# Kernel tuning notes

Measured on AMD Instinct MI355X. Metric: run time of the kernel, lower is better.

## Reference

```python
import jax, jax.numpy as jnp
import numpy as np

EMBED_DIM = 512
N_HEADS = 8
HEAD_DIM = EMBED_DIM // N_HEADS
B, S = 4, 2048

def gelu(x):
    # torch F.gelu default = exact erf gelu
    return jax.nn.gelu(x, approximate=False)

def setup_inputs() -> dict:
    key = jax.random.key(0)
    ks = jax.random.split(key, 9)
    sc = 1.0 / np.sqrt(EMBED_DIM)
    inp = {
        'x':   jax.random.normal(ks[0], (B, S, EMBED_DIM), dtype=jnp.float32),
        'Wq':  jax.random.uniform(ks[1], (EMBED_DIM, EMBED_DIM), jnp.float32, -sc, sc),
        'bq':  jax.random.uniform(ks[2], (EMBED_DIM,), jnp.float32, -sc, sc),
        'Wk':  jax.random.uniform(ks[3], (EMBED_DIM, EMBED_DIM), jnp.float32, -sc, sc),
        'bk':  jax.random.uniform(ks[4], (EMBED_DIM,), jnp.float32, -sc, sc),
        'Wv':  jax.random.uniform(ks[5], (EMBED_DIM, EMBED_DIM), jnp.float32, -sc, sc),
        'bv':  jax.random.uniform(ks[6], (EMBED_DIM,), jnp.float32, -sc, sc),
        'Wo':  jax.random.uniform(ks[7], (EMBED_DIM, EMBED_DIM), jnp.float32, -sc, sc),
        'bo':  jax.random.uniform(ks[8], (EMBED_DIM,), jnp.float32, -sc, sc),
    }
    return inp

def reference(x, Wq, bq, Wk, bk, Wv, bv, Wo, bo):
    Bsz, Ssz, _ = x.shape
    def proj(W, b):
        # [B,S,E] -> [B,H,S,D], GELU applied before head split (same math either way)
        h = gelu(jnp.einsum('bse,ef->bsf', x, W.T) + b)
        return h.reshape(Bsz, Ssz, N_HEADS, HEAD_DIM).transpose(0, 2, 1, 3)
    q = proj(Wq, bq)
    k = proj(Wk, bk)
    v = proj(Wv, bv)
    attn = jnp.einsum('bhid,bhjd->bhij', q, k) / np.sqrt(HEAD_DIM).astype(np.float32)
    attn = jax.nn.softmax(attn, axis=-1)
    o = jnp.einsum('bhij,bhjd->bhid', attn, v)
    o = o.transpose(0, 2, 1, 3).reshape(Bsz, Ssz, EMBED_DIM)
    return gelu(jnp.einsum('bse,ef->bsf', o, Wo.T) + bo)
```

## Files before the change

kernel.cpp:

```cpp
#include <hip/hip_runtime.h>
#include <hip/hip_bf16.h>

typedef __bf16 bf16_t;
typedef __bf16 bf16x4 __attribute__((ext_vector_type(4)));
typedef __bf16 bf16x8 __attribute__((ext_vector_type(8)));
typedef float  f32x4  __attribute__((ext_vector_type(4)));
typedef float  f32x8  __attribute__((ext_vector_type(8)));

#define EMBED 512
#define NH    8
#define HD    64
#define SEQ   2048
#define MTOT  8192
#define SCQ   0.18033688011112042f

__device__ __forceinline__ float gelu_f(float x) {
    return 0.5f * x * (1.0f + erff(x * 0.7071067811865475f));
}

__device__ __forceinline__ f32x4 mfma16(bf16x8 a, bf16x8 b, f32x4 c) {
    return __builtin_amdgcn_mfma_f32_16x16x32_bf16(a, b, c, 0, 0, 0);
}

__global__ __launch_bounds__(256)
void convert_kernel(const float* __restrict__ x,  const float* __restrict__ Wq,
                    const float* __restrict__ Wk, const float* __restrict__ Wv,
                    bf16_t* __restrict__ xb, bf16_t* __restrict__ wb)
{
    const int y = blockIdx.y;
    const float* src; bf16_t* dst;
    if (y < 16)      { src = x + (size_t)y * 262144; dst = xb + (size_t)y * 262144; }
    else if (y == 16){ src = Wq; dst = wb; }
    else if (y == 17){ src = Wk; dst = wb + 262144; }
    else             { src = Wv; dst = wb + 524288; }
    const int base = (blockIdx.x * 256 + threadIdx.x) * 16;
    const f32x8 a = *(const f32x8*)(src + base);
    const f32x8 b = *(const f32x8*)(src + base + 8);
    *(bf16x8*)(dst + base)     = __builtin_convertvector(a, bf16x8);
    *(bf16x8*)(dst + base + 8) = __builtin_convertvector(b, bf16x8);
}

template<int MODE, int NTILE>
__global__ __launch_bounds__(256, 3)
void gemm_gelu_kernel(const bf16_t* __restrict__ Xb,
                      const bf16_t* __restrict__ Wb,
                      const float*  __restrict__ Wf,
                      const float*  __restrict__ Bq, const float* __restrict__ Bk,
                      const float*  __restrict__ Bv,
                      bf16_t* __restrict__ O0, bf16_t* __restrict__ O1,
                      bf16_t* __restrict__ O2, float* __restrict__ Of)
{
    constexpr int NTN = NTILE / 32;
    __shared__ __align__(16) bf16_t As[128 * 72];
    __shared__ __align__(16) bf16_t Bs[NTILE * 72];
    const int tid  = threadIdx.x;
    const int lane = tid & 63, w = tid >> 6, quad = lane >> 4, l15 = lane & 15;
    const int m0 = blockIdx.x * 128;
    int mat, n0;
    if (MODE == 0) { mat = blockIdx.y >> 2; n0 = (blockIdx.y & 3) * NTILE; }
    else           { mat = 0;               n0 = blockIdx.y * NTILE; }
    const bf16_t* W  = (MODE == 0) ? (Wb + (size_t)mat * 262144) : nullptr;
    const float*  Bi = (MODE == 1) ? Bq : (mat == 0 ? Bq : (mat == 1 ? Bk : Bv));

    const int wr = (w >> 1) * 64;
    const int wc = (w & 1) * (NTILE / 2);

    const int srow = tid >> 3, scol = (tid & 7) * 8;

    f32x4 acc[4][NTN];
#pragma unroll
    for (int a = 0; a < 4; ++a)
#pragma unroll
        for (int b = 0; b < NTN; ++b) acc[a][b] = f32x4{0.f, 0.f, 0.f, 0.f};

    bf16x8 xp[4];
    bf16x8 wpb[NTN];
    f32x8  wpf[NTN];

#pragma unroll
    for (int it = 0; it < 4; ++it)
        xp[it] = *(const bf16x8*)(Xb + (size_t)(m0 + it * 32 + srow) * EMBED + scol);
#pragma unroll
    for (int it = 0; it < NTN; ++it) {
        const int r = it * 32 + srow;
        if (MODE == 0) wpb[it] = *(const bf16x8*)(W + (size_t)(n0 + r) * EMBED + scol);
        else           wpf[it] = *(const f32x8*)(Wf + (size_t)(n0 + r) * EMBED + scol);
    }

#pragma unroll 1
    for (int kt = 0; kt < 8; ++kt) {
        __syncthreads();
#pragma unroll
        for (int it = 0; it < 4; ++it)
            *(bf16x8*)(As + (it * 32 + srow) * 72 + scol) = xp[it];
#pragma unroll
        for (int it = 0; it < NTN; ++it) {
            const int r = it * 32 + srow;
            if (MODE == 0) *(bf16x8*)(Bs + r * 72 + scol) = wpb[it];
            else *(bf16x8*)(Bs + r * 72 + scol) = __builtin_convertvector(wpf[it], bf16x8);
        }
        if (kt < 7) {
            const int k1 = (kt + 1) * 64;
#pragma unroll
            for (int it = 0; it < 4; ++it)
                xp[it] = *(const bf16x8*)(Xb + (size_t)(m0 + it * 32 + srow) * EMBED + k1 + scol);
#pragma unroll
            for (int it = 0; it < NTN; ++it) {
                const int r = it * 32 + srow;
                if (MODE == 0) wpb[it] = *(const bf16x8*)(W + (size_t)(n0 + r) * EMBED + k1 + scol);
                else           wpf[it] = *(const f32x8*)(Wf + (size_t)(n0 + r) * EMBED + k1 + scol);
            }
        }
        __syncthreads();
#pragma unroll
        for (int ks = 0; ks < 2; ++ks) {
            const int ko = (ks * 4 + quad) * 8;
            bf16x8 av[4], bv[NTN];
#pragma unroll
            for (int mt = 0; mt < 4; ++mt)
                av[mt] = *(const bf16x8*)(As + (wr + mt * 16 + l15) * 72 + ko);
#pragma unroll
            for (int nt = 0; nt < NTN; ++nt)
                bv[nt] = *(const bf16x8*)(Bs + (wc + nt * 16 + l15) * 72 + ko);
#pragma unroll
            for (int mt = 0; mt < 4; ++mt)
#pragma unroll
                for (int nt = 0; nt < NTN; ++nt)
                    acc[mt][nt] = mfma16(av[mt], bv[nt], acc[mt][nt]);
        }
    }

    float biasv[NTN];
#pragma unroll
    for (int nt = 0; nt < NTN; ++nt)
        biasv[nt] = Bi[n0 + wc + nt * 16 + l15];
#pragma unroll
    for (int mt = 0; mt < 4; ++mt) {
        const int mb = m0 + wr + mt * 16 + quad * 4;
        const int bb = mb >> 11, s0 = mb & (SEQ - 1);
#pragma unroll
        for (int nt = 0; nt < NTN; ++nt) {
            const int fc = n0 + wc + nt * 16 + l15;
            const int h = fc >> 6, d = fc & 63;
            float vv[4];
#pragma unroll
            for (int i = 0; i < 4; ++i) vv[i] = gelu_f(acc[mt][nt][i] + biasv[nt]);
            if (MODE == 1) {
#pragma unroll
                for (int i = 0; i < 4; ++i) Of[(size_t)(mb + i) * EMBED + fc] = vv[i];
            } else if (mat == 0) {
#pragma unroll
                for (int i = 0; i < 4; ++i)
                    O0[(((size_t)(bb * NH + h)) * SEQ + s0 + i) * HD + d] = (bf16_t)(vv[i] * SCQ);
            } else if (mat == 1) {
#pragma unroll
                for (int i = 0; i < 4; ++i)
                    O1[(((size_t)(bb * NH + h)) * SEQ + s0 + i) * HD + d] = (bf16_t)vv[i];
            } else {
                bf16x4 pk;
#pragma unroll
                for (int i = 0; i < 4; ++i) pk[i] = (bf16_t)vv[i];
                *(bf16x4*)(O2 + ((size_t)(bb * NH + h) * HD + d) * SEQ + s0) = pk;
            }
        }
    }
}

__global__ __launch_bounds__(256, 3)
void flash_attn_kernel(const bf16_t* __restrict__ Q,
                       const bf16_t* __restrict__ K,
                       const bf16_t* __restrict__ Vt,
                       bf16_t* __restrict__ Og)
{
    __shared__ __align__(16) bf16_t Ks[2][64 * 72];
    __shared__ __align__(16) bf16_t Vs[2][64 * 72];
    __shared__ __align__(16) bf16_t Ps[4][16 * 72];

    const int tid  = threadIdx.x;
    const int lane = tid & 63, w = tid >> 6, quad = lane >> 4, l15 = lane & 15;
    const int bh = blockIdx.y;
    const int q0 = blockIdx.x * 64;
    const size_t baseQK = (size_t)bh * SEQ * HD;
    const size_t baseV  = (size_t)bh * HD * SEQ;
    const int wm = w * 16;

    bf16x8 qf[2];
#pragma unroll
    for (int ks = 0; ks < 2; ++ks)
        qf[ks] = *(const bf16x8*)(Q + baseQK + (size_t)(q0 + wm + l15) * HD + ks * 32 + quad * 8);

    float lsum = 0.f;
    f32x4 oacc[4];
#pragma unroll
    for (int nt = 0; nt < 4; ++nt) oacc[nt] = f32x4{0.f, 0.f, 0.f, 0.f};

    bf16_t* Pw = Ps[w];
    const int r0 = tid >> 3, c0 = (tid & 7) * 8;
    bf16x8 kr0, kr1, vr0, vr1;

    kr0 = *(const bf16x8*)(K + baseQK + (size_t)r0 * HD + c0);
    kr1 = *(const bf16x8*)(K + baseQK + (size_t)(r0 + 32) * HD + c0);
    vr0 = *(const bf16x8*)(Vt + baseV + (size_t)r0 * SEQ + c0);
    vr1 = *(const bf16x8*)(Vt + baseV + (size_t)(r0 + 32) * SEQ + c0);
    *(bf16x8*)(Ks[0] + r0 * 72 + c0)        = kr0;
    *(bf16x8*)(Ks[0] + (r0 + 32) * 72 + c0) = kr1;
    *(bf16x8*)(Vs[0] + r0 * 72 + c0)        = vr0;
    *(bf16x8*)(Vs[0] + (r0 + 32) * 72 + c0) = vr1;
    kr0 = *(const bf16x8*)(K + baseQK + (size_t)(64 + r0) * HD + c0);
    kr1 = *(const bf16x8*)(K + baseQK + (size_t)(64 + r0 + 32) * HD + c0);
    vr0 = *(const bf16x8*)(Vt + baseV + (size_t)r0 * SEQ + 64 + c0);
    vr1 = *(const bf16x8*)(Vt + baseV + (size_t)(r0 + 32) * SEQ + 64 + c0);

#pragma unroll 1
    for (int t = 0; t < 32; ++t) {
        __syncthreads();
        if (t + 1 < 32) {
            bf16_t* Kn = Ks[(t + 1) & 1];
            bf16_t* Vn = Vs[(t + 1) & 1];
            *(bf16x8*)(Kn + r0 * 72 + c0)        = kr0;
            *(bf16x8*)(Kn + (r0 + 32) * 72 + c0) = kr1;
            *(bf16x8*)(Vn + r0 * 72 + c0)        = vr0;
            *(bf16x8*)(Vn + (r0 + 32) * 72 + c0) = vr1;
        }
        if (t + 2 < 32) {
            const int kv = (t + 2) * 64;
            kr0 = *(const bf16x8*)(K + baseQK + (size_t)(kv + r0) * HD + c0);
            kr1 = *(const bf16x8*)(K + baseQK + (size_t)(kv + r0 + 32) * HD + c0);
            vr0 = *(const bf16x8*)(Vt + baseV + (size_t)r0 * SEQ + kv + c0);
            vr1 = *(const bf16x8*)(Vt + baseV + (size_t)(r0 + 32) * SEQ + kv + c0);
        }

        const bf16_t* Kb = Ks[t & 1];
        const bf16_t* Vb = Vs[t & 1];

        f32x4 sf[4];
#pragma unroll
        for (int jt = 0; jt < 4; ++jt) sf[jt] = f32x4{0.f, 0.f, 0.f, 0.f};
#pragma unroll
        for (int ks = 0; ks < 2; ++ks) {
            const int ko = ks * 32 + quad * 8;
#pragma unroll
            for (int jt = 0; jt < 4; ++jt) {
                const bf16x8 a = *(const bf16x8*)(Kb + (jt * 16 + l15) * 72 + ko);
                sf[jt] = mfma16(a, qf[ks], sf[jt]);
            }
        }

#pragma unroll
        for (int jt = 0; jt < 4; ++jt) {
#pragma unroll
            for (int i = 0; i < 4; ++i) {
                const float pv = exp2f(sf[jt][i] - 8.f);
                sf[jt][i] = pv;
                lsum += pv;
            }
            const bf16x4 pk = __builtin_convertvector(sf[jt], bf16x4);
            *(bf16x4*)(Pw + l15 * 72 + jt * 16 + quad * 4) = pk;
        }

#pragma unroll
        for (int c = 0; c < 2; ++c) {
            const int ko = c * 32 + quad * 8;
            const bf16x8 a = *(const bf16x8*)(Pw + l15 * 72 + ko);
#pragma unroll
            for (int nt = 0; nt < 4; ++nt) {
                const bf16x8 b = *(const bf16x8*)(Vb + (nt * 16 + l15) * 72 + ko);
                oacc[nt] = mfma16(a, b, oacc[nt]);
            }
        }
    }

    float rs = lsum;
    rs += __shfl_xor(rs, 16);
    rs += __shfl_xor(rs, 32);
    const int bidx = bh >> 3, h = bh & 7;
    float lf[4];
#pragma unroll
    for (int i = 0; i < 4; ++i)
        lf[i] = __shfl(rs, (lane & 48) | (quad * 4 + i));
#pragma unroll
    for (int nt = 0; nt < 4; ++nt)
#pragma unroll
        for (int i = 0; i < 4; ++i) {
            const int s = q0 + wm + quad * 4 + i;
            const int d = nt * 16 + l15;
            Og[((size_t)(bidx * SEQ + s)) * EMBED + h * HD + d] =
                (bf16_t)(oacc[nt][i] / lf[i]);
        }
}

extern "C" void kernel_launch(void* const* d_in, const int* in_sizes, int n_in,
                              void* d_out, int out_size, void* d_ws, size_t ws_size,
                              hipStream_t stream)
{
    const float* x  = (const float*)d_in[0];
    const float* Wq = (const float*)d_in[1];
    const float* bq = (const float*)d_in[2];
    const float* Wk = (const float*)d_in[3];
    const float* bk = (const float*)d_in[4];
    const float* Wv = (const float*)d_in[5];
    const float* bv = (const float*)d_in[6];
    const float* Wo = (const float*)d_in[7];
    const float* bo = (const float*)d_in[8];
    float* out = (float*)d_out;

    const size_t NE = (size_t)MTOT * EMBED;
    bf16_t* xb  = (bf16_t*)d_out;
    bf16_t* Qw  = (bf16_t*)d_out + NE;
    bf16_t* Kw  = (bf16_t*)d_ws;
    bf16_t* Vtw = Kw + NE;
    bf16_t* Ow  = Vtw + NE;
    bf16_t* Wb  = Ow;

    convert_kernel<<<dim3(64, 19), 256, 0, stream>>>(x, Wq, Wk, Wv, xb, Wb);
    gemm_gelu_kernel<0, 128><<<dim3(64, 12), 256, 0, stream>>>(
        xb, Wb, nullptr, bq, bk, bv, Qw, Kw, Vtw, nullptr);
    flash_attn_kernel<<<dim3(32, 32), 256, 0, stream>>>(Qw, Kw, Vtw, Ow);
    gemm_gelu_kernel<1, 64><<<dim3(64, 8), 256, 0, stream>>>(
        Ow, nullptr, Wo, bo, nullptr, nullptr, nullptr, nullptr, nullptr, out);
}
```

Measured before the change: 190.7 us.

## Keep attention P in registers via shuffles and vectorize projection and output stores

The attention kernel no longer writes the softmax probabilities to shared memory. It rebuilds the bf16 operand with cross-lane shuffles and swaps the MFMA operand order, so the output accumulator comes out transposed and the final store can be a 4-wide vector. Removing the P buffer cuts shared memory use, and launch bounds are raised to 4 blocks per SM. The Q/K projection also swaps MFMA operands so its epilogue can write packed bf16x4 and load a float4 bias. A side change drops the constant -8 offset in exp2, which could raise overflow risk, and the extra shuffles add VALU work per tile.

After: 288.4 us. 1.51x slower.

```diff
diff --git a/kernel.cpp b/kernel.cpp
--- a/kernel.cpp
+++ b/kernel.cpp
@@ -21,6 +21,9 @@
 __device__ __forceinline__ f32x4 mfma16(bf16x8 a, bf16x8 b, f32x4 c) {
     return __builtin_amdgcn_mfma_f32_16x16x32_bf16(a, b, c, 0, 0, 0);
 }
+
+union U2 { bf16x4 v; uint2 u; };
+union U4 { bf16x8 v; int   x[4]; };
 
 __global__ __launch_bounds__(256)
 void convert_kernel(const float* __restrict__ x,  const float* __restrict__ Wq,
@@ -61,10 +64,10 @@
     else           { mat = 0;               n0 = blockIdx.y * NTILE; }
     const bf16_t* W  = (MODE == 0) ? (Wb + (size_t)mat * 262144) : nullptr;
     const float*  Bi = (MODE == 1) ? Bq : (mat == 0 ? Bq : (mat == 1 ? Bk : Bv));
+    const bool swp = (MODE == 0) && (mat < 2);
 
     const int wr = (w >> 1) * 64;
     const int wc = (w & 1) * (NTILE / 2);
-
     const int srow = tid >> 3, scol = (tid & 7) * 8;
 
     f32x4 acc[4][NTN];
@@ -122,51 +125,75 @@
 #pragma unroll
             for (int nt = 0; nt < NTN; ++nt)
                 bv[nt] = *(const bf16x8*)(Bs + (wc + nt * 16 + l15) * 72 + ko);
-#pragma unroll
-            for (int mt = 0; mt < 4; ++mt)
-#pragma unroll
-                for (int nt = 0; nt < NTN; ++nt)
-                    acc[mt][nt] = mfma16(av[mt], bv[nt], acc[mt][nt]);
-        }
-    }
-
-    float biasv[NTN];
-#pragma unroll
-    for (int nt = 0; nt < NTN; ++nt)
-        biasv[nt] = Bi[n0 + wc + nt * 16 + l15];
-#pragma unroll
-    for (int mt = 0; mt < 4; ++mt) {
-        const int mb = m0 + wr + mt * 16 + quad * 4;
-        const int bb = mb >> 11, s0 = mb & (SEQ - 1);
-#pragma unroll
-        for (int nt = 0; nt < NTN; ++nt) {
-            const int fc = n0 + wc + nt * 16 + l15;
-            const int h = fc >> 6, d = fc & 63;
-            float vv[4];
-#pragma unroll
-            for (int i = 0; i < 4; ++i) vv[i] = gelu_f(acc[mt][nt][i] + biasv[nt]);
-            if (MODE == 1) {
-#pragma unroll
-                for (int i = 0; i < 4; ++i) Of[(size_t)(mb + i) * EMBED + fc] = vv[i];
-            } else if (mat == 0) {
+            if (swp) {
+#pragma unroll
+                for (int a = 0; a < NTN; ++a)
+#pragma unroll
+                    for (int b = 0; b < 4; ++b)
+                        acc[a][b] = mfma16(bv[a], av[b], acc[a][b]);
+            } else {
+#pragma unroll
+                for (int a = 0; a < 4; ++a)
+#pragma unroll
+                    for (int b = 0; b < NTN; ++b)
+                        acc[a][b] = mfma16(av[a], bv[b], acc[a][b]);
+            }
+        }
+    }
+
+    if (MODE == 0 && mat < 2) {
+        bf16_t* O = (mat == 0) ? O0 : O1;
+        const float scl = (mat == 0) ? SCQ : 1.0f;
+#pragma unroll
+        for (int at = 0; at < 4; ++at) {
+            const int nb = n0 + wc + at * 16 + quad * 4;
+            const int h = nb >> 6, d0 = nb & 63;
+            const f32x4 b4 = *(const f32x4*)(Bi + nb);
+#pragma unroll
+            for (int bt = 0; bt < 4; ++bt) {
+                const int m = m0 + wr + bt * 16 + l15;
+                const int bb = m >> 11, s = m & (SEQ - 1);
+                bf16x4 pk;
 #pragma unroll
                 for (int i = 0; i < 4; ++i)
-                    O0[(((size_t)(bb * NH + h)) * SEQ + s0 + i) * HD + d] = (bf16_t)(vv[i] * SCQ);
-            } else if (mat == 1) {
+                    pk[i] = (bf16_t)(gelu_f(acc[at][bt][i] + b4[i]) * scl);
+                *(bf16x4*)(O + (((size_t)(bb * NH + h)) * SEQ + s) * HD + d0) = pk;
+            }
+        }
+    } else if (MODE == 0) {
+#pragma unroll
+        for (int mt = 0; mt < 4; ++mt) {
+            const int mb = m0 + wr + mt * 16 + quad * 4;
+            const int bb = mb >> 11, s0 = mb & (SEQ - 1);
+#pragma unroll
+            for (int nt = 0; nt < 4; ++nt) {
+                const int fc = n0 + wc + nt * 16 + l15;
+                const int h = fc >> 6, d = fc & 63;
+                const float bs = Bi[fc];
+                bf16x4 pk;
 #pragma unroll
                 for (int i = 0; i < 4; ++i)
-                    O1[(((size_t)(bb * NH + h)) * SEQ + s0 + i) * HD + d] = (bf16_t)vv[i];
-            } else {
-                bf16x4 pk;
-#pragma unroll
-                for (int i = 0; i < 4; ++i) pk[i] = (bf16_t)vv[i];
+                    pk[i] = (bf16_t)gelu_f(acc[mt][nt][i] + bs);
                 *(bf16x4*)(O2 + ((size_t)(bb * NH + h) * HD + d) * SEQ + s0) = pk;
             }
         }
-    }
-}
-
-__global__ __launch_bounds__(256, 3)
+    } else {
+#pragma unroll
+        for (int mt = 0; mt < 4; ++mt) {
+            const int mb = m0 + wr + mt * 16 + quad * 4;
+#pragma unroll
+            for (int nt = 0; nt < NTN; ++nt) {
+                const int fc = n0 + wc + nt * 16 + l15;
+                const float bs = Bi[fc];
+#pragma unroll
+                for (int i = 0; i < 4; ++i)
+                    Of[(size_t)(mb + i) * EMBED + fc] = gelu_f(acc[mt][nt][i] + bs);
+            }
+        }
+    }
+}
+
+__global__ __launch_bounds__(256, 4)
 void flash_attn_kernel(const bf16_t* __restrict__ Q,
                        const bf16_t* __restrict__ K,
                        const bf16_t* __restrict__ Vt,
@@ -174,7 +201,6 @@
 {
     __shared__ __align__(16) bf16_t Ks[2][64 * 72];
     __shared__ __align__(16) bf16_t Vs[2][64 * 72];
-    __shared__ __align__(16) bf16_t Ps[4][16 * 72];
 
     const int tid  = threadIdx.x;
     const int lane = tid & 63, w = tid >> 6, quad = lane >> 4, l15 = lane & 15;
@@ -194,7 +220,6 @@
 #pragma unroll
     for (int nt = 0; nt < 4; ++nt) oacc[nt] = f32x4{0.f, 0.f, 0.f, 0.f};
 
-    bf16_t* Pw = Ps[w];
     const int r0 = tid >> 3, c0 = (tid & 7) * 8;
     bf16x8 kr0, kr1, vr0, vr1;
 
@@ -211,6 +236,10 @@
     vr0 = *(const bf16x8*)(Vt + baseV + (size_t)r0 * SEQ + 64 + c0);
     vr1 = *(const bf16x8*)(Vt + baseV + (size_t)(r0 + 32) * SEQ + 64 + c0);
 
+    const int lA = (((quad * 2) & 3) << 4) | l15;
+    const int lB = (((quad * 2 + 1) & 3) << 4) | l15;
+    const bool hiq = quad >= 2;
+
 #pragma unroll 1
     for (int t = 0; t < 32; ++t) {
         __syncthreads();
@@ -246,26 +275,39 @@
             }
         }
 
+        uint2 pk[4];
 #pragma unroll
         for (int jt = 0; jt < 4; ++jt) {
+            f32x4 p;
 #pragma unroll
             for (int i = 0; i < 4; ++i) {
-                const float pv = exp2f(sf[jt][i] - 8.f);
-                sf[jt][i] = pv;
-                lsum += pv;
-            }
-            const bf16x4 pk = __builtin_convertvector(sf[jt], bf16x4);
-            *(bf16x4*)(Pw + l15 * 72 + jt * 16 + quad * 4) = pk;
+                p[i] = exp2f(sf[jt][i]);
+                lsum += p[i];
+            }
+            U2 u; u.v = __builtin_convertvector(p, bf16x4);
+            pk[jt] = u.u;
         }
 
 #pragma unroll
         for (int c = 0; c < 2; ++c) {
+            const int a0 = __shfl((int)pk[2 * c].x, lA);
+            const int a1 = __shfl((int)pk[2 * c].y, lA);
+            const int a2 = __shfl((int)pk[2 * c].x, lB);
+            const int a3 = __shfl((int)pk[2 * c].y, lB);
+            const int b0 = __shfl((int)pk[2 * c + 1].x, lA);
+            const int b1 = __shfl((int)pk[2 * c + 1].y, lA);
+            const int b2 = __shfl((int)pk[2 * c + 1].x, lB);
+            const int b3 = __shfl((int)pk[2 * c + 1].y, lB);
+            U4 bu;
+            bu.x[0] = hiq ? b0 : a0;
+            bu.x[1] = hiq ? b1 : a1;
+            bu.x[2] = hiq ? b2 : a2;
+            bu.x[3] = hiq ? b3 : a3;
             const int ko = c * 32 + quad * 8;
-            const bf16x8 a = *(const bf16x8*)(Pw + l15 * 72 + ko);
 #pragma unroll
             for (int nt = 0; nt < 4; ++nt) {
-                const bf16x8 b = *(const bf16x8*)(Vb + (nt * 16 + l15) * 72 + ko);
-                oacc[nt] = mfma16(a, b, oacc[nt]);
+                const bf16x8 va = *(const bf16x8*)(Vb + (nt * 16 + l15) * 72 + ko);
+                oacc[nt] = mfma16(va, bu.v, oacc[nt]);
             }
         }
     }
@@ -273,20 +315,17 @@
     float rs = lsum;
     rs += __shfl_xor(rs, 16);
     rs += __shfl_xor(rs, 32);
+    const float inv = 1.0f / rs;
     const int bidx = bh >> 3, h = bh & 7;
-    float lf[4];
-#pragma unroll
-    for (int i = 0; i < 4; ++i)
-        lf[i] = __shfl(rs, (lane & 48) | (quad * 4 + i));
-#pragma unroll
-    for (int nt = 0; nt < 4; ++nt)
-#pragma unroll
-        for (int i = 0; i < 4; ++i) {
-            const int s = q0 + wm + quad * 4 + i;
-            const int d = nt * 16 + l15;
-            Og[((size_t)(bidx * SEQ + s)) * EMBED + h * HD + d] =
-                (bf16_t)(oacc[nt][i] / lf[i]);
-        }
+    const int s = q0 + wm + l15;
+    bf16_t* orow = Og + ((size_t)(bidx * SEQ + s)) * EMBED + h * HD;
+#pragma unroll
+    for (int nt = 0; nt < 4; ++nt) {
+        bf16x4 o4;
+#pragma unroll
+        for (int i = 0; i < 4; ++i) o4[i] = (bf16_t)(oacc[nt][i] * inv);
+        *(bf16x4*)(orow + nt * 16 + quad * 4) = o4;
+    }
 }
 
 extern "C" void kernel_launch(void* const* d_in, const int* in_sizes, int n_in,
```

## Stage QKV projection epilogue through shared memory for coalesced 16-byte stores

Applied to the files above, without the earlier changes.

The QKV projection epilogue now writes GELU outputs into a shared-memory tile (reusing the A/B staging buffers) and then writes them to global memory as contiguous bf16x8 rows. Previously Q and K were stored as scattered 2-byte values and V as 8-byte chunks. For Q and K the MFMA operand order is swapped so each lane holds consecutive columns, which allows packed LDS writes and vectorised bias loads. This removes uncoalesced global stores at the cost of two extra barriers and an LDS round trip. The epilogue assumes a 128-wide N tile in mode 0.

Result: slower. 277.2 us (+45.3%).

```diff
diff --git a/kernel.cpp b/kernel.cpp
--- a/kernel.cpp
+++ b/kernel.cpp
@@ -51,8 +51,9 @@
                       bf16_t* __restrict__ O2, float* __restrict__ Of)
 {
     constexpr int NTN = NTILE / 32;
-    __shared__ __align__(16) bf16_t As[128 * 72];
-    __shared__ __align__(16) bf16_t Bs[NTILE * 72];
+    __shared__ __align__(16) bf16_t SMEM[128 * 72 + NTILE * 72];
+    bf16_t* As = SMEM;
+    bf16_t* Bs = SMEM + 128 * 72;
     const int tid  = threadIdx.x;
     const int lane = tid & 63, w = tid >> 6, quad = lane >> 4, l15 = lane & 15;
     const int m0 = blockIdx.x * 128;
@@ -61,10 +62,10 @@
     else           { mat = 0;               n0 = blockIdx.y * NTILE; }
     const bf16_t* W  = (MODE == 0) ? (Wb + (size_t)mat * 262144) : nullptr;
     const float*  Bi = (MODE == 1) ? Bq : (mat == 0 ? Bq : (mat == 1 ? Bk : Bv));
+    const bool swp = (MODE == 0) && (mat < 2);
 
     const int wr = (w >> 1) * 64;
     const int wc = (w & 1) * (NTILE / 2);
-
     const int srow = tid >> 3, scol = (tid & 7) * 8;
 
     f32x4 acc[4][NTN];
@@ -122,45 +123,90 @@
 #pragma unroll
             for (int nt = 0; nt < NTN; ++nt)
                 bv[nt] = *(const bf16x8*)(Bs + (wc + nt * 16 + l15) * 72 + ko);
-#pragma unroll
-            for (int mt = 0; mt < 4; ++mt)
-#pragma unroll
-                for (int nt = 0; nt < NTN; ++nt)
-                    acc[mt][nt] = mfma16(av[mt], bv[nt], acc[mt][nt]);
+            if (swp) {
+#pragma unroll
+                for (int a = 0; a < NTN; ++a)
+#pragma unroll
+                    for (int b = 0; b < 4; ++b)
+                        acc[a][b] = mfma16(bv[a], av[b], acc[a][b]);
+            } else {
+#pragma unroll
+                for (int a = 0; a < 4; ++a)
+#pragma unroll
+                    for (int b = 0; b < NTN; ++b)
+                        acc[a][b] = mfma16(av[a], bv[b], acc[a][b]);
+            }
         }
     }
 
-    float biasv[NTN];
-#pragma unroll
-    for (int nt = 0; nt < NTN; ++nt)
-        biasv[nt] = Bi[n0 + wc + nt * 16 + l15];
-#pragma unroll
-    for (int mt = 0; mt < 4; ++mt) {
-        const int mb = m0 + wr + mt * 16 + quad * 4;
-        const int bb = mb >> 11, s0 = mb & (SEQ - 1);
-#pragma unroll
-        for (int nt = 0; nt < NTN; ++nt) {
-            const int fc = n0 + wc + nt * 16 + l15;
-            const int h = fc >> 6, d = fc & 63;
-            float vv[4];
-#pragma unroll
-            for (int i = 0; i < 4; ++i) vv[i] = gelu_f(acc[mt][nt][i] + biasv[nt]);
-            if (MODE == 1) {
-#pragma unroll
-                for (int i = 0; i < 4; ++i) Of[(size_t)(mb + i) * EMBED + fc] = vv[i];
-            } else if (mat == 0) {
+    if (MODE == 0) {
+        bf16_t* T = SMEM;
+        __syncthreads();
+        if (swp) {
+            const float scl = (mat == 0) ? SCQ : 1.0f;
+#pragma unroll
+            for (int at = 0; at < 4; ++at) {
+                const int nb = wc + at * 16 + quad * 4;
+                const f32x4 b4 = *(const f32x4*)(Bi + n0 + nb);
+#pragma unroll
+                for (int bt = 0; bt < 4; ++bt) {
+                    const int m = wr + bt * 16 + l15;
+                    bf16x4 pk;
+#pragma unroll
+                    for (int i = 0; i < 4; ++i)
+                        pk[i] = (bf16_t)(gelu_f(acc[at][bt][i] + b4[i]) * scl);
+                    *(bf16x4*)(T + m * 136 + nb) = pk;
+                }
+            }
+        } else {
+#pragma unroll
+            for (int mt = 0; mt < 4; ++mt) {
+                const int mloc = wr + mt * 16 + quad * 4;
+#pragma unroll
+                for (int nt = 0; nt < 4; ++nt) {
+                    const int nloc = wc + nt * 16 + l15;
+                    const float bs = Bi[n0 + nloc];
+                    bf16x4 pk;
+#pragma unroll
+                    for (int i = 0; i < 4; ++i)
+                        pk[i] = (bf16_t)gelu_f(acc[mt][nt][i] + bs);
+                    *(bf16x4*)(T + nloc * 136 + mloc) = pk;
+                }
+            }
+        }
+        __syncthreads();
+        const int row = tid & 127, half = tid >> 7;
+        if (mat < 2) {
+            bf16_t* O = (mat == 0) ? O0 : O1;
+            const int m = m0 + row, bb = m >> 11, s = m & (SEQ - 1);
+#pragma unroll
+            for (int j = 0; j < 8; ++j) {
+                const int dl = half * 64 + j * 8;
+                const bf16x8 v = *(const bf16x8*)(T + row * 136 + dl);
+                const int fc = n0 + dl, h = fc >> 6, d = fc & 63;
+                *(bf16x8*)(O + (((size_t)(bb * NH + h)) * SEQ + s) * HD + d) = v;
+            }
+        } else {
+            const int fc = n0 + row, h = fc >> 6, d = fc & 63;
+#pragma unroll
+            for (int j = 0; j < 8; ++j) {
+                const int ml = half * 64 + j * 8;
+                const bf16x8 v = *(const bf16x8*)(T + row * 136 + ml);
+                const int m = m0 + ml, bb = m >> 11, s0 = m & (SEQ - 1);
+                *(bf16x8*)(O2 + ((size_t)(bb * NH + h) * HD + d) * SEQ + s0) = v;
+            }
+        }
+    } else {
+#pragma unroll
+        for (int mt = 0; mt < 4; ++mt) {
+            const int mb = m0 + wr + mt * 16 + quad * 4;
+#pragma unroll
+            for (int nt = 0; nt < NTN; ++nt) {
+                const int fc = n0 + wc + nt * 16 + l15;
+                const float bs = Bi[fc];
 #pragma unroll
                 for (int i = 0; i < 4; ++i)
-                    O0[(((size_t)(bb * NH + h)) * SEQ + s0 + i) * HD + d] = (bf16_t)(vv[i] * SCQ);
-            } else if (mat == 1) {
-#pragma unroll
-                for (int i = 0; i < 4; ++i)
-                    O1[(((size_t)(bb * NH + h)) * SEQ + s0 + i) * HD + d] = (bf16_t)vv[i];
-            } else {
-                bf16x4 pk;
-#pragma unroll
-                for (int i = 0; i < 4; ++i) pk[i] = (bf16_t)vv[i];
-                *(bf16x4*)(O2 + ((size_t)(bb * NH + h) * HD + d) * SEQ + s0) = pk;
+                    Of[(size_t)(mb + i) * EMBED + fc] = gelu_f(acc[mt][nt][i] + bs);
             }
         }
     }
```
